# Optimization experiments

Hardware: AMD Instinct MI355X
Metric: run time of the kernel (lower is better)

Reference implementation:

```python
import jax, jax.numpy as jnp
import numpy as np

EPS = float(np.finfo(np.float32).eps)
SEQ_LEN = 2048
NUM_HEADS = 16
DIM_EMB = 1024
DIM_HEAD = DIM_EMB // NUM_HEADS
DIM_K = DIM_EMB  # module scales by full dim_k, not per-head dim
BATCH = 2


def cosine_positional_encoding(seq_len, dim):
    idx = jnp.arange(seq_len, dtype=jnp.float32)
    scale = 1.0 / (10000.0 ** (jnp.arange(0, dim, 2, dtype=jnp.float32) / dim) + EPS)
    ang = idx[:, None] * scale[None, :]  # [S, dim/2]
    # interleave sin (even) and cos (odd) along last dim -> [S, dim]
    return jnp.stack([jnp.sin(ang), jnp.cos(ang)], axis=-1).reshape(seq_len, dim)


def setup_inputs() -> dict:
    key = jax.random.key(0)
    ks = jax.random.split(key, 5)
    s = DIM_EMB ** -0.5
    return {
        "x": jax.random.normal(ks[0], (BATCH, SEQ_LEN, DIM_EMB), dtype=jnp.float32),
        "Wq": jax.random.normal(ks[1], (DIM_EMB, DIM_EMB), dtype=jnp.float32) * s,
        "Wk": jax.random.normal(ks[2], (DIM_EMB, DIM_EMB), dtype=jnp.float32) * s,
        "Wv": jax.random.normal(ks[3], (DIM_EMB, DIM_EMB), dtype=jnp.float32) * s,
        "Wo": jax.random.normal(ks[4], (DIM_EMB, DIM_EMB), dtype=jnp.float32) * s,
    }


def reference(x, Wq, Wk, Wv, Wo):
    B, S, E = x.shape
    pos = cosine_positional_encoding(S, DIM_HEAD)  # [S, dim_head]
    # projections (bias-free)
    def split_heads(t):
        return t.reshape(B, S, NUM_HEADS, DIM_HEAD).transpose(0, 2, 1, 3)  # [B,H,S,D]
    q = split_heads(x @ Wq) + pos[None, None]
    k = split_heads(x @ Wk) + pos[None, None]
    v = split_heads(x @ Wv)
    scores = jnp.einsum("bhqd,bhkd->bhqk", q, k) * (DIM_K ** -0.5)
    causal_mask = jnp.triu(jnp.ones((S, S), dtype=bool), k=1)
    m_inf = -jnp.finfo(scores.dtype).max
    scores = jnp.where(causal_mask[None, None], m_inf, scores)
    attn = jax.nn.softmax(scores, axis=-1)
    out = jnp.einsum("bhqk,bhkd->bhqd", attn, v)
    out = out.transpose(0, 2, 1, 3).reshape(B, S, E)
    return out @ Wo
```

## Files before the change

kernel.cpp:

```cpp
#include <hip/hip_runtime.h>
#include <math.h>

#define BATCH 2
#define SEQ   2048
#define EMB   1024
#define NHEAD 16
#define DHEAD 64
#define MROWS (BATCH*SEQ)
#define QKS   2048

typedef unsigned int  uint;
typedef unsigned short ushort;
typedef __attribute__((ext_vector_type(8))) short short8;
typedef __attribute__((ext_vector_type(4))) float f32x4;

__device__ __forceinline__ float exp2_fast(float x) {
    return __builtin_amdgcn_exp2f(x);
}

__global__ void pos_init(float* __restrict__ pos) {
    int s = blockIdx.x;
    int d = threadIdx.x;
    int i = d >> 1;
    float expo  = (float)(2 * i) / (float)DHEAD;
    float scale = 1.0f / (powf(10000.0f, expo) + 1.1920928955078125e-07f);
    float ang   = (float)s * scale;
    pos[s * DHEAD + d] = (d & 1) ? cosf(ang) : sinf(ang);
}

__device__ __forceinline__ uint pack_bf16x2(float a, float b) {
    union { float f; uint u; } x, y;
    x.f = a; y.f = b;
    uint ua = x.u + 0x7fffu + ((x.u >> 16) & 1u);
    uint ub = y.u + 0x7fffu + ((y.u >> 16) & 1u);
    return (ua >> 16) | (ub & 0xffff0000u);
}
__device__ __forceinline__ ushort bf16_1(float a) {
    union { float f; uint u; } x; x.f = a;
    return (ushort)((x.u + 0x7fffu + ((x.u >> 16) & 1u)) >> 16);
}

__device__ __forceinline__ void gll16(const ushort* g, ushort* l) {
    __builtin_amdgcn_global_load_lds(
        (const __attribute__((address_space(1))) uint*)g,
        (__attribute__((address_space(3))) uint*)l, 16, 0, 0);
}

__global__ __launch_bounds__(256) void cvt_bf16(
    const float* __restrict__ in, ushort* __restrict__ out, int n2) {
    int gid = blockIdx.x * 256 + threadIdx.x;
    if (gid < n2) {
        float2 v = ((const float2*)in)[gid];
        ((uint*)out)[gid] = pack_bf16x2(v.x, v.y);
    }
}

__global__ __launch_bounds__(256) void wt_bf16_all(
    const float* __restrict__ Wq, const float* __restrict__ Wk,
    const float* __restrict__ Wv, const float* __restrict__ Wo,
    ushort* __restrict__ Wqkvt, ushort* __restrict__ Wot) {
    __shared__ float tile[32][33];
    const int which = blockIdx.z;
    const float* W = (which == 0) ? Wq : (which == 1) ? Wk : (which == 2) ? Wv : Wo;
    ushort* Wt = (which < 3) ? (Wqkvt + (size_t)which * 1024 * EMB) : Wot;
    const int c0 = blockIdx.x * 32;
    const int r0 = blockIdx.y * 32;
    const int tx = threadIdx.x & 31;
    const int ty = threadIdx.x >> 5;
#pragma unroll
    for (int i = 0; i < 4; ++i)
        tile[ty + i * 8][tx] = W[(size_t)(r0 + ty + i * 8) * EMB + c0 + tx];
    __syncthreads();
#pragma unroll
    for (int i = 0; i < 4; ++i)
        Wt[(size_t)(c0 + ty + i * 8) * EMB + r0 + tx] = bf16_1(tile[tx][ty + i * 8]);
}

#define TK 32
#define SCLQ (0.03125f * 1.44269504088896f)

template<int TMT>
__global__ __launch_bounds__(256) void gemm_mfma_t(
    const ushort* __restrict__ A, const ushort* __restrict__ Bt,
    void* __restrict__ Cv, ushort* __restrict__ VtOut,
    const float* __restrict__ pos, int posmode, int N, int K) {
    constexpr int MI = TMT / 32;
    __shared__ ushort As[TMT * TK];
    __shared__ ushort Bs[128 * TK];

    const int t    = threadIdx.x;
    const int lane = t & 63, w = t >> 6;
    const int quad = lane >> 4, l15 = lane & 15;
    const int bm = blockIdx.x * TMT, bn = blockIdx.y * 128;
    const int wm = (w & 1) * (TMT / 2), wn = (w >> 1) * 64;
    const int r0 = t >> 2, kp = (t & 3) * 8;

    f32x4 acc[MI][4];
#pragma unroll
    for (int mi = 0; mi < MI; ++mi)
#pragma unroll
        for (int ni = 0; ni < 4; ++ni)
            acc[mi][ni] = (f32x4){0.f, 0.f, 0.f, 0.f};

    for (int k0 = 0; k0 < K; k0 += TK) {
        __syncthreads();
#pragma unroll
        for (int i = 0; i < TMT / 64; ++i)
            gll16(A + (size_t)(bm + i * 64 + r0) * K + k0 + kp, &As[i * 2048 + t * 8]);
#pragma unroll
        for (int i = 0; i < 2; ++i)
            gll16(Bt + (size_t)(bn + i * 64 + r0) * K + k0 + kp, &Bs[i * 2048 + t * 8]);
        __syncthreads();

        short8 af[MI], bfv[4];
#pragma unroll
        for (int mi = 0; mi < MI; ++mi)
            af[mi] = *(const short8*)&As[(wm + mi * 16 + l15) * TK + quad * 8];
#pragma unroll
        for (int ni = 0; ni < 4; ++ni)
            bfv[ni] = *(const short8*)&Bs[(wn + ni * 16 + l15) * TK + quad * 8];
#pragma unroll
        for (int mi = 0; mi < MI; ++mi)
#pragma unroll
            for (int ni = 0; ni < 4; ++ni)
                acc[mi][ni] = __builtin_amdgcn_mfma_f32_16x16x32_bf16(
                    af[mi], bfv[ni], acc[mi][ni], 0, 0, 0);
    }

#pragma unroll
    for (int mi = 0; mi < MI; ++mi) {
        const int row0 = bm + wm + mi * 16 + quad * 4;
#pragma unroll
        for (int ni = 0; ni < 4; ++ni) {
            const int col = bn + wn + ni * 16 + l15;
            if (!posmode) {
#pragma unroll
                for (int r = 0; r < 4; ++r)
                    ((float*)Cv)[(size_t)(row0 + r) * N + col] = acc[mi][ni][r];
            } else if (col < 2048) {
#pragma unroll
                for (int r = 0; r < 4; ++r) {
                    const int row = row0 + r;
                    const int s   = row & (SEQ - 1);
                    float v = acc[mi][ni][r] + pos[s * DHEAD + (col & 63)];
                    if (col < 1024) v *= SCLQ;
                    ((ushort*)Cv)[(size_t)row * QKS + col] = bf16_1(v);
                }
            } else {
                const int hh = (col >> 6) & 15;
                const int d  = col & 63;
                const int bb = row0 >> 11;
                const int s0 = row0 & (SEQ - 1);
                uint2 u;
                u.x = pack_bf16x2(acc[mi][ni][0], acc[mi][ni][1]);
                u.y = pack_bf16x2(acc[mi][ni][2], acc[mi][ni][3]);
                *(uint2*)&VtOut[((size_t)(bb * 16 + hh) * 64 + d) * SEQ + s0] = u;
            }
        }
    }
}

#define LDP 72

__global__ __launch_bounds__(256) void attn_mfma7(
    const ushort* __restrict__ QK, const ushort* __restrict__ Vt,
    ushort* __restrict__ AOb) {
    __shared__ ushort Ks[64 * LDP];
    __shared__ ushort Vs[64 * LDP];
    __shared__ ushort Ps[64 * LDP];

    const int pair = blockIdx.x;
    const int bh   = blockIdx.y;
    const int b    = bh >> 4, hd = bh & 15;
    const int t    = threadIdx.x;
    const int lane = t & 63, w = t >> 6;
    const int quad = lane >> 4, l15 = lane & 15;
    const int wrow = w * 16;
    const int sr = t >> 2;
    const int sc = (t & 3) * 16;

    const size_t qkbase = (size_t)b * SEQ * QKS + hd * 64;
    const ushort* kpb = QK + qkbase + 1024 + (size_t)sr * QKS + sc;
    const ushort* vpb = Vt + ((size_t)bh * 64 + sr) * SEQ;

#pragma unroll
    for (int ph = 0; ph < 2; ++ph) {
        const int qt = ph ? (31 - pair) : pair;

        const ushort* qp = QK + qkbase + (size_t)(qt * 64 + wrow + l15) * QKS + quad * 8;
        const short8 aq0 = *(const short8*)qp;
        const short8 aq1 = *(const short8*)(qp + 32);

        uint4 ka = *(const uint4*)kpb;
        uint4 kb = *(const uint4*)(kpb + 8);
        uint4 va = *(const uint4*)(vpb + sc);
        uint4 vb = *(const uint4*)(vpb + sc + 8);

        f32x4 acc_o[4];
#pragma unroll
        for (int nd = 0; nd < 4; ++nd) acc_o[nd] = (f32x4){0.f, 0.f, 0.f, 0.f};
        float m_l = -3.0e38f, l_l = 0.f;
        const int qrow_g = qt * 64 + wrow + l15;

        for (int kt = 0; kt <= qt; ++kt) {
            __syncthreads();
            *(uint4*)&Ks[sr * LDP + sc]     = ka;
            *(uint4*)&Ks[sr * LDP + sc + 8] = kb;
            *(uint4*)&Vs[sr * LDP + sc]     = va;
            *(uint4*)&Vs[sr * LDP + sc + 8] = vb;
            const int ktn = (kt < qt) ? kt + 1 : qt;
            ka = *(const uint4*)(kpb + (size_t)ktn * 64 * QKS);
            kb = *(const uint4*)(kpb + (size_t)ktn * 64 * QKS + 8);
            va = *(const uint4*)(vpb + ktn * 64 + sc);
            vb = *(const uint4*)(vpb + ktn * 64 + sc + 8);
            __syncthreads();

            float sv[4][4];
            float mloc = m_l;
            const bool diag = (kt == qt);
#pragma unroll
            for (int kg = 0; kg < 4; ++kg) {
                const short8 ak0 = *(const short8*)&Ks[(kg * 16 + l15) * LDP + quad * 8];
                const short8 ak1 = *(const short8*)&Ks[(kg * 16 + l15) * LDP + 32 + quad * 8];
                f32x4 a = (f32x4){0.f, 0.f, 0.f, 0.f};
                a = __builtin_amdgcn_mfma_f32_16x16x32_bf16(ak0, aq0, a, 0, 0, 0);
                a = __builtin_amdgcn_mfma_f32_16x16x32_bf16(ak1, aq1, a, 0, 0, 0);
                const int keyb = kt * 64 + kg * 16 + quad * 4;
#pragma unroll
                for (int r = 0; r < 4; ++r) {
                    float v = a[r];
                    if (diag && (keyb + r > qrow_g)) v = -3.0e38f;
                    sv[kg][r] = v;
                    mloc = fmaxf(mloc, v);
                }
            }
            mloc = fmaxf(mloc, __shfl_xor(mloc, 16, 64));
            mloc = fmaxf(mloc, __shfl_xor(mloc, 32, 64));
            const float alpha = exp2_fast(m_l - mloc);
            m_l = mloc;
            float rs = 0.f;
#pragma unroll
            for (int kg = 0; kg < 4; ++kg)
#pragma unroll
                for (int r = 0; r < 4; ++r) {
                    float p = exp2_fast(sv[kg][r] - mloc);
                    sv[kg][r] = p;
                    rs += p;
                }
            rs += __shfl_xor(rs, 16, 64);
            rs += __shfl_xor(rs, 32, 64);
            l_l = l_l * alpha + rs;

            float av[4];
#pragma unroll
            for (int r = 0; r < 4; ++r) av[r] = __shfl(alpha, quad * 4 + r, 64);
#pragma unroll
            for (int nd = 0; nd < 4; ++nd)
#pragma unroll
                for (int r = 0; r < 4; ++r) acc_o[nd][r] *= av[r];

            ushort* Pw = &Ps[wrow * LDP];
#pragma unroll
            for (int kg = 0; kg < 4; ++kg) {
                uint2 u;
                u.x = pack_bf16x2(sv[kg][0], sv[kg][1]);
                u.y = pack_bf16x2(sv[kg][2], sv[kg][3]);
                *(uint2*)&Pw[l15 * LDP + kg * 16 + quad * 4] = u;
            }
            const short8 pa0 = *(const short8*)&Pw[l15 * LDP + quad * 8];
            const short8 pa1 = *(const short8*)&Pw[l15 * LDP + 32 + quad * 8];
#pragma unroll
            for (int nd = 0; nd < 4; ++nd) {
                const short8 bv0 = *(const short8*)&Vs[(nd * 16 + l15) * LDP + quad * 8];
                const short8 bv1 = *(const short8*)&Vs[(nd * 16 + l15) * LDP + 32 + quad * 8];
                acc_o[nd] = __builtin_amdgcn_mfma_f32_16x16x32_bf16(pa0, bv0, acc_o[nd], 0, 0, 0);
                acc_o[nd] = __builtin_amdgcn_mfma_f32_16x16x32_bf16(pa1, bv1, acc_o[nd], 0, 0, 0);
            }
        }

        float linv[4];
#pragma unroll
        for (int r = 0; r < 4; ++r) linv[r] = 1.0f / __shfl(l_l, quad * 4 + r, 64);
#pragma unroll
        for (int nd = 0; nd < 4; ++nd)
#pragma unroll
            for (int r = 0; r < 4; ++r) {
                const int row = qt * 64 + wrow + quad * 4 + r;
                AOb[(size_t)(b * SEQ + row) * EMB + hd * 64 + nd * 16 + l15] =
                    bf16_1(acc_o[nd][r] * linv[r]);
            }
    }
}

#define BM 64
#define BN 64
#define BK 16

__global__ __launch_bounds__(256) void gemm_f32(
    const float* __restrict__ A, const float* __restrict__ B,
    float* __restrict__ C, const float* __restrict__ pos, int addpos,
    int M, int N, int K) {
    __shared__ float As[BK][BM];
    __shared__ float Bs[BK][BN];
    const int tid = threadIdx.x;
    const int bm  = blockIdx.x * BM;
    const int bn  = blockIdx.y * BN;
    const int tx  = tid & 15;
    const int ty  = tid >> 4;
    const int arow = tid >> 2;
    const int acol = (tid & 3) << 2;
    const int brow = tid >> 4;
    const int bcol = (tid & 15) << 2;
    float acc[4][4] = {{0.f}};
    const float* Aptr = A + (size_t)(bm + arow) * K + acol;
    const float* Bptr = B + (size_t)brow * N + bn + bcol;
    for (int k0 = 0; k0 < K; k0 += BK) {
        float4 av = *(const float4*)(Aptr + k0);
        float4 bv = *(const float4*)(Bptr + (size_t)k0 * N);
        __syncthreads();
        As[acol + 0][arow] = av.x;
        As[acol + 1][arow] = av.y;
        As[acol + 2][arow] = av.z;
        As[acol + 3][arow] = av.w;
        *(float4*)&Bs[brow][bcol] = bv;
        __syncthreads();
#pragma unroll
        for (int kk = 0; kk < BK; ++kk) {
            float4 a = *(const float4*)&As[kk][ty << 2];
            float4 b = *(const float4*)&Bs[kk][tx << 2];
            float aa[4] = {a.x, a.y, a.z, a.w};
            float bb[4] = {b.x, b.y, b.z, b.w};
#pragma unroll
            for (int i = 0; i < 4; ++i)
#pragma unroll
                for (int j = 0; j < 4; ++j)
                    acc[i][j] += aa[i] * bb[j];
        }
    }
#pragma unroll
    for (int i = 0; i < 4; ++i) {
        int m = bm + (ty << 2) + i;
        int n = bn + (tx << 2);
        float4 v = make_float4(acc[i][0], acc[i][1], acc[i][2], acc[i][3]);
        if (addpos) {
            int s = m & (SEQ - 1);
            int d = n & (DHEAD - 1);
            float4 p = *(const float4*)&pos[s * DHEAD + d];
            v.x += p.x; v.y += p.y; v.z += p.z; v.w += p.w;
        }
        *(float4*)&C[(size_t)m * N + n] = v;
    }
}

#define QT 128
#define KT 32
__global__ __launch_bounds__(QT) void attn_fwd(
    const float* __restrict__ Q, const float* __restrict__ Kg,
    const float* __restrict__ V, float* __restrict__ O) {
    __shared__ float Ks[KT][DHEAD];
    __shared__ float Vs[KT][DHEAD];
    const int t    = threadIdx.x;
    const int q0   = blockIdx.x * QT;
    const int bh   = blockIdx.y;
    const int b    = bh >> 4;
    const int h    = bh & 15;
    const int qrow = q0 + t;
    const size_t base = (size_t)b * SEQ * EMB + (size_t)h * DHEAD;
    float4 q4[16], o4[16];
#pragma unroll
    for (int i = 0; i < 16; ++i) {
        q4[i] = *(const float4*)&Q[base + (size_t)qrow * EMB + i * 4];
        o4[i] = make_float4(0.f, 0.f, 0.f, 0.f);
    }
    float m_i = -3.0e38f, l_i = 0.0f;
    const float scale = 0.03125f;
    const int kend = q0 + QT;
    for (int k0 = 0; k0 < kend; k0 += KT) {
        __syncthreads();
#pragma unroll
        for (int i = 0; i < 4; ++i) {
            int idx = t + i * QT;
            int r = idx >> 4;
            int c = (idx & 15) << 2;
            *(float4*)&Ks[r][c] = *(const float4*)&Kg[base + (size_t)(k0 + r) * EMB + c];
            *(float4*)&Vs[r][c] = *(const float4*)&V [base + (size_t)(k0 + r) * EMB + c];
        }
        __syncthreads();
        float sv[KT];
        float mt = m_i;
#pragma unroll
        for (int j = 0; j < KT; ++j) {
            const float4* kr = (const float4*)Ks[j];
            float dot = 0.f;
#pragma unroll
            for (int dd = 0; dd < 16; ++dd) {
                float4 kv = kr[dd];
                dot += q4[dd].x * kv.x + q4[dd].y * kv.y +
                       q4[dd].z * kv.z + q4[dd].w * kv.w;
            }
            sv[j] = (k0 + j <= qrow) ? dot * scale : -3.0e38f;
            mt = fmaxf(mt, sv[j]);
        }
        float corr = __expf(m_i - mt);
        l_i *= corr;
#pragma unroll
        for (int i = 0; i < 16; ++i) {
            o4[i].x *= corr; o4[i].y *= corr; o4[i].z *= corr; o4[i].w *= corr;
        }
#pragma unroll
        for (int j = 0; j < KT; ++j) {
            float pp = __expf(sv[j] - mt);
            l_i += pp;
            const float4* vr = (const float4*)Vs[j];
#pragma unroll
            for (int dd = 0; dd < 16; ++dd) {
                float4 vv = vr[dd];
                o4[dd].x += pp * vv.x; o4[dd].y += pp * vv.y;
                o4[dd].z += pp * vv.z; o4[dd].w += pp * vv.w;
            }
        }
        m_i = mt;
    }
    float inv = 1.0f / l_i;
#pragma unroll
    for (int i = 0; i < 16; ++i) {
        float4 v = o4[i];
        v.x *= inv; v.y *= inv; v.z *= inv; v.w *= inv;
        *(float4*)&O[base + (size_t)qrow * EMB + i * 4] = v;
    }
}

extern "C" void kernel_launch(void* const* d_in, const int* in_sizes, int n_in,
                              void* d_out, int out_size, void* d_ws, size_t ws_size,
                              hipStream_t stream) {
    const float* x  = (const float*)d_in[0];
    const float* Wq = (const float*)d_in[1];
    const float* Wk = (const float*)d_in[2];
    const float* Wv = (const float*)d_in[3];
    const float* Wo = (const float*)d_in[4];
    float* out = (float*)d_out;

    char* ws = (char*)d_ws;
    size_t off = 0;
    float*  pos   = (float*)(ws + off);  off += (size_t)SEQ * DHEAD * 4;
    ushort* xb    = (ushort*)(ws + off); off += (size_t)MROWS * EMB * 2;
    ushort* Wqkvt = (ushort*)(ws + off); off += (size_t)3072 * EMB * 2;
    ushort* Wot   = (ushort*)(ws + off); off += (size_t)EMB * EMB * 2;
    ushort* QKb   = (ushort*)(ws + off); off += (size_t)MROWS * QKS * 2;
    ushort* Vtp   = (ushort*)(ws + off); off += (size_t)MROWS * EMB * 2;
    ushort* AOb   = (ushort*)(ws + off); off += (size_t)MROWS * EMB * 2;
    const bool use_bf16 = off <= ws_size;

    const int M = MROWS, K = EMB;

    pos_init<<<SEQ, DHEAD, 0, stream>>>(pos);

    if (use_bf16) {
        const int n2 = MROWS * EMB / 2;
        cvt_bf16<<<n2 / 256, 256, 0, stream>>>(x, xb, n2);
        wt_bf16_all<<<dim3(EMB / 32, EMB / 32, 4), 256, 0, stream>>>(
            Wq, Wk, Wv, Wo, Wqkvt, Wot);

        gemm_mfma_t<128><<<dim3(M / 128, 3072 / 128), 256, 0, stream>>>(
            xb, Wqkvt, QKb, Vtp, pos, 1, 3072, K);

        attn_mfma7<<<dim3(16, BATCH * NHEAD), 256, 0, stream>>>(QKb, Vtp, AOb);

        gemm_mfma_t<64><<<dim3(M / 64, EMB / 128), 256, 0, stream>>>(
            AOb, Wot, out, nullptr, pos, 0, EMB, K);
    } else {
        size_t f = 0;
        float* posf = (float*)(ws + f); f += (size_t)SEQ * DHEAD * 4;
        float* Qb = (float*)(ws + f); f += (size_t)MROWS * EMB * 4;
        float* Kb = (float*)(ws + f); f += (size_t)MROWS * EMB * 4;
        float* Vb = (float*)(ws + f); f += (size_t)MROWS * EMB * 4;
        float* AO = (float*)(ws + f);
        dim3 g(M / BM, EMB / BN);
        gemm_f32<<<g, 256, 0, stream>>>(x, Wq, Qb, posf, 1, M, EMB, K);
        gemm_f32<<<g, 256, 0, stream>>>(x, Wk, Kb, posf, 1, M, EMB, K);
        gemm_f32<<<g, 256, 0, stream>>>(x, Wv, Vb, posf, 0, M, EMB, K);
        attn_fwd<<<dim3(SEQ / QT, BATCH * NHEAD), QT, 0, stream>>>(Qb, Kb, Vb, AO);
        gemm_f32<<<g, 256, 0, stream>>>(AO, Wo, out, posf, 0, M, EMB, K);
    }
}
```

Baseline: 198.6 us.

## Launch one attention block per query tile with heavy-first ordering and lazy rescale

The attention kernel now launches 1024 blocks, one per (batch-head, query tile), ordered so the longest causal tiles run first. Before, each block processed a light and a heavy tile as a pair. The online softmax only rescales the accumulator when the running max grows by more than 8 (in log2 units), which skips most alpha multiplies. It also uses the hardware packed bf16 convert and raises wave priority around the MFMA sections. The goal is better load balance across CUs and less VALU work per key tile. In exchange, each block reloads its Q tile, and the lazy rescale relies on the fp32 range being large enough to absorb the skipped normalisation.

```diff
diff --git a/kernel.cpp b/kernel.cpp
--- a/kernel.cpp
+++ b/kernel.cpp
@@ -38,6 +38,11 @@
 __device__ __forceinline__ ushort bf16_1(float a) {
     union { float f; uint u; } x; x.f = a;
     return (ushort)((x.u + 0x7fffu + ((x.u >> 16) & 1u)) >> 16);
+}
+__device__ __forceinline__ uint cvt_pk_bf16(float lo, float hi) {
+    uint r;
+    asm("v_cvt_pk_bf16_f32 %0, %1, %2" : "=v"(r) : "v"(lo), "v"(hi));
+    return r;
 }
 
 __device__ __forceinline__ void gll16(const ushort* g, ushort* l) {
@@ -162,15 +167,16 @@
 
 #define LDP 72
 
-__global__ __launch_bounds__(256) void attn_mfma7(
+__global__ __launch_bounds__(256) void attn_mfma8(
     const ushort* __restrict__ QK, const ushort* __restrict__ Vt,
     ushort* __restrict__ AOb) {
     __shared__ ushort Ks[64 * LDP];
     __shared__ ushort Vs[64 * LDP];
     __shared__ ushort Ps[64 * LDP];
 
-    const int pair = blockIdx.x;
-    const int bh   = blockIdx.y;
+    const int bid  = blockIdx.x;
+    const int bh   = (bid & 7) + ((bid >> 8) << 3);
+    const int qt   = 31 - ((bid >> 3) & 31);
     const int b    = bh >> 4, hd = bh & 15;
     const int t    = threadIdx.x;
     const int lane = t & 63, w = t >> 6;
@@ -183,74 +189,63 @@
     const ushort* kpb = QK + qkbase + 1024 + (size_t)sr * QKS + sc;
     const ushort* vpb = Vt + ((size_t)bh * 64 + sr) * SEQ;
 
-#pragma unroll
-    for (int ph = 0; ph < 2; ++ph) {
-        const int qt = ph ? (31 - pair) : pair;
-
-        const ushort* qp = QK + qkbase + (size_t)(qt * 64 + wrow + l15) * QKS + quad * 8;
-        const short8 aq0 = *(const short8*)qp;
-        const short8 aq1 = *(const short8*)(qp + 32);
-
-        uint4 ka = *(const uint4*)kpb;
-        uint4 kb = *(const uint4*)(kpb + 8);
-        uint4 va = *(const uint4*)(vpb + sc);
-        uint4 vb = *(const uint4*)(vpb + sc + 8);
-
-        f32x4 acc_o[4];
-#pragma unroll
-        for (int nd = 0; nd < 4; ++nd) acc_o[nd] = (f32x4){0.f, 0.f, 0.f, 0.f};
-        float m_l = -3.0e38f, l_l = 0.f;
-        const int qrow_g = qt * 64 + wrow + l15;
-
-        for (int kt = 0; kt <= qt; ++kt) {
-            __syncthreads();
-            *(uint4*)&Ks[sr * LDP + sc]     = ka;
-            *(uint4*)&Ks[sr * LDP + sc + 8] = kb;
-            *(uint4*)&Vs[sr * LDP + sc]     = va;
-            *(uint4*)&Vs[sr * LDP + sc + 8] = vb;
-            const int ktn = (kt < qt) ? kt + 1 : qt;
-            ka = *(const uint4*)(kpb + (size_t)ktn * 64 * QKS);
-            kb = *(const uint4*)(kpb + (size_t)ktn * 64 * QKS + 8);
-            va = *(const uint4*)(vpb + ktn * 64 + sc);
-            vb = *(const uint4*)(vpb + ktn * 64 + sc + 8);
-            __syncthreads();
-
-            float sv[4][4];
-            float mloc = m_l;
-            const bool diag = (kt == qt);
-#pragma unroll
-            for (int kg = 0; kg < 4; ++kg) {
-                const short8 ak0 = *(const short8*)&Ks[(kg * 16 + l15) * LDP + quad * 8];
-                const short8 ak1 = *(const short8*)&Ks[(kg * 16 + l15) * LDP + 32 + quad * 8];
-                f32x4 a = (f32x4){0.f, 0.f, 0.f, 0.f};
-                a = __builtin_amdgcn_mfma_f32_16x16x32_bf16(ak0, aq0, a, 0, 0, 0);
-                a = __builtin_amdgcn_mfma_f32_16x16x32_bf16(ak1, aq1, a, 0, 0, 0);
-                const int keyb = kt * 64 + kg * 16 + quad * 4;
-#pragma unroll
-                for (int r = 0; r < 4; ++r) {
-                    float v = a[r];
-                    if (diag && (keyb + r > qrow_g)) v = -3.0e38f;
-                    sv[kg][r] = v;
-                    mloc = fmaxf(mloc, v);
-                }
+    const ushort* qp = QK + qkbase + (size_t)(qt * 64 + wrow + l15) * QKS + quad * 8;
+    const short8 aq0 = *(const short8*)qp;
+    const short8 aq1 = *(const short8*)(qp + 32);
+
+    uint4 ka = *(const uint4*)kpb;
+    uint4 kb = *(const uint4*)(kpb + 8);
+    uint4 va = *(const uint4*)(vpb + sc);
+    uint4 vb = *(const uint4*)(vpb + sc + 8);
+
+    f32x4 acc_o[4];
+#pragma unroll
+    for (int nd = 0; nd < 4; ++nd) acc_o[nd] = (f32x4){0.f, 0.f, 0.f, 0.f};
+    float m_l = -3.0e38f, l_l = 0.f;
+    const int qrow_g = qt * 64 + wrow + l15;
+
+    for (int kt = 0; kt <= qt; ++kt) {
+        __syncthreads();
+        *(uint4*)&Ks[sr * LDP + sc]     = ka;
+        *(uint4*)&Ks[sr * LDP + sc + 8] = kb;
+        *(uint4*)&Vs[sr * LDP + sc]     = va;
+        *(uint4*)&Vs[sr * LDP + sc + 8] = vb;
+        const int ktn = (kt < qt) ? kt + 1 : qt;
+        ka = *(const uint4*)(kpb + (size_t)ktn * 64 * QKS);
+        kb = *(const uint4*)(kpb + (size_t)ktn * 64 * QKS + 8);
+        va = *(const uint4*)(vpb + ktn * 64 + sc);
+        vb = *(const uint4*)(vpb + ktn * 64 + sc + 8);
+        __syncthreads();
+
+        float sv[4][4];
+        float pmax = -3.0e38f;
+        const bool diag = (kt == qt);
+        __builtin_amdgcn_s_setprio(1);
+#pragma unroll
+        for (int kg = 0; kg < 4; ++kg) {
+            const short8 ak0 = *(const short8*)&Ks[(kg * 16 + l15) * LDP + quad * 8];
+            const short8 ak1 = *(const short8*)&Ks[(kg * 16 + l15) * LDP + 32 + quad * 8];
+            f32x4 a = (f32x4){0.f, 0.f, 0.f, 0.f};
+            a = __builtin_amdgcn_mfma_f32_16x16x32_bf16(ak0, aq0, a, 0, 0, 0);
+            a = __builtin_amdgcn_mfma_f32_16x16x32_bf16(ak1, aq1, a, 0, 0, 0);
+            const int keyb = kt * 64 + kg * 16 + quad * 4;
+#pragma unroll
+            for (int r = 0; r < 4; ++r) {
+                float v = a[r];
+                if (diag && (keyb + r > qrow_g)) v = -3.0e38f;
+                sv[kg][r] = v;
+                pmax = fmaxf(pmax, v);
             }
-            mloc = fmaxf(mloc, __shfl_xor(mloc, 16, 64));
-            mloc = fmaxf(mloc, __shfl_xor(mloc, 32, 64));
-            const float alpha = exp2_fast(m_l - mloc);
-            m_l = mloc;
-            float rs = 0.f;
-#pragma unroll
-            for (int kg = 0; kg < 4; ++kg)
-#pragma unroll
-                for (int r = 0; r < 4; ++r) {
-                    float p = exp2_fast(sv[kg][r] - mloc);
-                    sv[kg][r] = p;
-                    rs += p;
-                }
-            rs += __shfl_xor(rs, 16, 64);
-            rs += __shfl_xor(rs, 32, 64);
-            l_l = l_l * alpha + rs;
-
+        }
+        __builtin_amdgcn_s_setprio(0);
+        pmax = fmaxf(pmax, __shfl_xor(pmax, 16, 64));
+        pmax = fmaxf(pmax, __shfl_xor(pmax, 32, 64));
+
+        if (__any(pmax - m_l > 8.f)) {
+            const float m_new = fmaxf(m_l, pmax);
+            const float alpha = exp2_fast(m_l - m_new);
+            m_l = m_new;
+            l_l *= alpha;
             float av[4];
 #pragma unroll
             for (int r = 0; r < 4; ++r) av[r] = __shfl(alpha, quad * 4 + r, 64);
@@ -258,38 +253,53 @@
             for (int nd = 0; nd < 4; ++nd)
 #pragma unroll
                 for (int r = 0; r < 4; ++r) acc_o[nd][r] *= av[r];
-
-            ushort* Pw = &Ps[wrow * LDP];
-#pragma unroll
-            for (int kg = 0; kg < 4; ++kg) {
-                uint2 u;
-                u.x = pack_bf16x2(sv[kg][0], sv[kg][1]);
-                u.y = pack_bf16x2(sv[kg][2], sv[kg][3]);
-                *(uint2*)&Pw[l15 * LDP + kg * 16 + quad * 4] = u;
+        }
+
+        float rs = 0.f;
+#pragma unroll
+        for (int kg = 0; kg < 4; ++kg)
+#pragma unroll
+            for (int r = 0; r < 4; ++r) {
+                float p = exp2_fast(sv[kg][r] - m_l);
+                sv[kg][r] = p;
+                rs += p;
             }
-            const short8 pa0 = *(const short8*)&Pw[l15 * LDP + quad * 8];
-            const short8 pa1 = *(const short8*)&Pw[l15 * LDP + 32 + quad * 8];
-#pragma unroll
-            for (int nd = 0; nd < 4; ++nd) {
-                const short8 bv0 = *(const short8*)&Vs[(nd * 16 + l15) * LDP + quad * 8];
-                const short8 bv1 = *(const short8*)&Vs[(nd * 16 + l15) * LDP + 32 + quad * 8];
-                acc_o[nd] = __builtin_amdgcn_mfma_f32_16x16x32_bf16(pa0, bv0, acc_o[nd], 0, 0, 0);
-                acc_o[nd] = __builtin_amdgcn_mfma_f32_16x16x32_bf16(pa1, bv1, acc_o[nd], 0, 0, 0);
-            }
-        }
-
-        float linv[4];
-#pragma unroll
-        for (int r = 0; r < 4; ++r) linv[r] = 1.0f / __shfl(l_l, quad * 4 + r, 64);
-#pragma unroll
-        for (int nd = 0; nd < 4; ++nd)
-#pragma unroll
-            for (int r = 0; r < 4; ++r) {
-                const int row = qt * 64 + wrow + quad * 4 + r;
-                AOb[(size_t)(b * SEQ + row) * EMB + hd * 64 + nd * 16 + l15] =
-                    bf16_1(acc_o[nd][r] * linv[r]);
-            }
-    }
+        rs += __shfl_xor(rs, 16, 64);
+        rs += __shfl_xor(rs, 32, 64);
+        l_l += rs;
+
+        ushort* Pw = &Ps[wrow * LDP];
+#pragma unroll
+        for (int kg = 0; kg < 4; ++kg) {
+            uint2 u;
+            u.x = cvt_pk_bf16(sv[kg][0], sv[kg][1]);
+            u.y = cvt_pk_bf16(sv[kg][2], sv[kg][3]);
+            *(uint2*)&Pw[l15 * LDP + kg * 16 + quad * 4] = u;
+        }
+        const short8 pa0 = *(const short8*)&Pw[l15 * LDP + quad * 8];
+        const short8 pa1 = *(const short8*)&Pw[l15 * LDP + 32 + quad * 8];
+        __builtin_amdgcn_s_setprio(1);
+#pragma unroll
+        for (int nd = 0; nd < 4; ++nd) {
+            const short8 bv0 = *(const short8*)&Vs[(nd * 16 + l15) * LDP + quad * 8];
+            const short8 bv1 = *(const short8*)&Vs[(nd * 16 + l15) * LDP + 32 + quad * 8];
+            acc_o[nd] = __builtin_amdgcn_mfma_f32_16x16x32_bf16(pa0, bv0, acc_o[nd], 0, 0, 0);
+            acc_o[nd] = __builtin_amdgcn_mfma_f32_16x16x32_bf16(pa1, bv1, acc_o[nd], 0, 0, 0);
+        }
+        __builtin_amdgcn_s_setprio(0);
+    }
+
+    float linv[4];
+#pragma unroll
+    for (int r = 0; r < 4; ++r) linv[r] = 1.0f / __shfl(l_l, quad * 4 + r, 64);
+#pragma unroll
+    for (int nd = 0; nd < 4; ++nd)
+#pragma unroll
+        for (int r = 0; r < 4; ++r) {
+            const int row = qt * 64 + wrow + quad * 4 + r;
+            AOb[(size_t)(b * SEQ + row) * EMB + hd * 64 + nd * 16 + l15] =
+                bf16_1(acc_o[nd][r] * linv[r]);
+        }
 }
 
 #define BM 64
@@ -464,7 +474,7 @@
         gemm_mfma_t<128><<<dim3(M / 128, 3072 / 128), 256, 0, stream>>>(
             xb, Wqkvt, QKb, Vtp, pos, 1, 3072, K);
 
-        attn_mfma7<<<dim3(16, BATCH * NHEAD), 256, 0, stream>>>(QKb, Vtp, AOb);
+        attn_mfma8<<<dim3(1024), 256, 0, stream>>>(QKb, Vtp, AOb);
 
         gemm_mfma_t<64><<<dim3(M / 64, EMB / 128), 256, 0, stream>>>(
             AOb, Wot, out, nullptr, pos, 0, EMB, K);
```

Result: slower. 213.4 us (+7.5%).
